# Kernel tuning notes

Hardware: AMD Instinct MI355X
Metric: run time of the kernel (lower is better)

Reference implementation:

```python
import jax, jax.numpy as jnp
import numpy as np

B, S, D, H = 2, 2048, 1024, 16
DK = D // H


def setup_inputs() -> dict:
    key = jax.random.key(0)
    ks = jax.random.split(key, 11)
    scale = 1.0 / np.sqrt(D)
    inp = {
        'q': jax.random.normal(ks[0], (B, S, D), jnp.float32),
        'k': jax.random.normal(ks[1], (B, S, D), jnp.float32),
        'v': jax.random.normal(ks[2], (B, S, D), jnp.float32),
        'mask': jnp.tril(jnp.ones((S, S), jnp.int32))[None, None],  # [1,1,S,S] causal
        'w_q': jax.random.normal(ks[3], (D, D), jnp.float32) * scale,
        'b_q': jax.random.normal(ks[4], (D,), jnp.float32) * scale,
        'w_k': jax.random.normal(ks[5], (D, D), jnp.float32) * scale,
        'b_k': jax.random.normal(ks[6], (D,), jnp.float32) * scale,
        'w_v': jax.random.normal(ks[7], (D, D), jnp.float32) * scale,
        'b_v': jax.random.normal(ks[8], (D,), jnp.float32) * scale,
        'w_o': jax.random.normal(ks[9], (D, D), jnp.float32) * scale,
        'b_o': jax.random.normal(ks[10], (D,), jnp.float32) * scale,
    }
    return inp


def reference(q, k, v, mask, w_q, b_q, w_k, b_k, w_v, b_v, w_o, b_o):
    # Linear projections (torch Linear: x @ W^T + b; here weights stored as [D_in, D_out])
    query = q @ w_q + b_q  # [B,S,D]
    key_ = k @ w_k + b_k
    value = v @ w_v + b_v
    # split heads -> [B,H,S,DK]
    def split(x):
        return x.reshape(B, S, H, DK).transpose(0, 2, 1, 3)
    qh, kh, vh = split(query), split(key_), split(value)
    scores = jnp.einsum('bhqd,bhkd->bhqk', qh, kh) / jnp.sqrt(jnp.float32(DK))
    scores = jnp.where(mask == 0, jnp.float32(-1e9), scores)
    attn = jax.nn.softmax(scores, axis=-1)  # dropout p=0.0 -> identity
    out = jnp.einsum('bhqk,bhkd->bhqd', attn, vh)  # [B,H,S,DK]
    out = out.transpose(0, 2, 1, 3).reshape(B, S, D)
    return out @ w_o + b_o
```

## Files before the change

kernel.cpp:

```cpp
#include <hip/hip_runtime.h>

typedef unsigned short u16;
typedef unsigned int u32;
typedef __attribute__((ext_vector_type(8))) short short8;
typedef __attribute__((ext_vector_type(4))) float f32x4;
typedef __attribute__((ext_vector_type(4))) float float4v;
typedef __attribute__((ext_vector_type(4))) u16 u16x4;
typedef __attribute__((ext_vector_type(2))) u32 u32x2;

#define DEV static __device__ __forceinline__

static constexpr int S_LEN = 2048;
static constexpr int D_MODEL = 1024;
static constexpr int N_HEADS = 16;
static constexpr int DK = 64;
static constexpr float LOG2E = 1.4426950408889634f;
static constexpr float SM_SHIFT = 12.0f;

#if defined(__has_builtin)
#if __has_builtin(__builtin_amdgcn_exp2f)
#define EXP2(x) __builtin_amdgcn_exp2f(x)
#else
#define EXP2(x) exp2f(x)
#endif
#else
#define EXP2(x) exp2f(x)
#endif

DEV u16 f2bf(float f) {
  u32 u = __builtin_bit_cast(u32, f);
  u32 r = (u + 0x7FFFu + ((u >> 16) & 1u)) >> 16;
  return (u16)r;
}

DEV u32 pk2bf(float lo, float hi) {
  u32 d;
  asm("v_cvt_pk_bf16_f32 %0, %1, %2" : "=v"(d) : "v"(lo), "v"(hi));
  return d;
}

DEV void async16(const void* g, void* l) {
  __builtin_amdgcn_global_load_lds(
      (const __attribute__((address_space(1))) u32*)g,
      (__attribute__((address_space(3))) u32*)l, 16, 0, 0);
}

DEV short8 lds_frag(const u16* tile, int row, int byteInRow) {
  const char* p = (const char*)tile + row * 128 + (byteInRow ^ ((row & 7) << 4));
  return *(const short8*)p;
}

DEV f32x4 mfma16(short8 a, short8 b, f32x4 c) {
  return __builtin_amdgcn_mfma_f32_16x16x32_bf16(a, b, c, 0, 0, 0);
}

__global__ void k_cvt3(const float* __restrict__ q, const float* __restrict__ k,
                       const float* __restrict__ v, u16* __restrict__ xq,
                       u16* __restrict__ xk, u16* __restrict__ xv, int n) {
  const float* src = blockIdx.y == 0 ? q : (blockIdx.y == 1 ? k : v);
  u16* dst = blockIdx.y == 0 ? xq : (blockIdx.y == 1 ? xk : xv);
  int i = (blockIdx.x * blockDim.x + threadIdx.x) * 4;
  int stride = gridDim.x * blockDim.x * 4;
  for (; i < n; i += stride) {
    float4v f = *(const float4v*)(src + i);
    u16x4 o;
    o[0] = f2bf(f[0]); o[1] = f2bf(f[1]); o[2] = f2bf(f[2]); o[3] = f2bf(f[3]);
    *(u16x4*)(dst + i) = o;
  }
}

__global__ void k_twz4(const float* __restrict__ wq, const float* __restrict__ wk,
                       const float* __restrict__ wv, const float* __restrict__ wo,
                       u16* __restrict__ tq, u16* __restrict__ tk,
                       u16* __restrict__ tv, u16* __restrict__ to_) {
  __shared__ u16 t[64][65];
  const int z = blockIdx.z;
  const float* W = z == 0 ? wq : (z == 1 ? wk : (z == 2 ? wv : wo));
  u16* Wt = z == 0 ? tq : (z == 1 ? tk : (z == 2 ? tv : to_));
  const int n0 = blockIdx.x * 64;
  const int k0 = blockIdx.y * 64;
  const int tid = threadIdx.x;
  const int c = tid & 63, r0 = tid >> 6;
#pragma unroll
  for (int j = 0; j < 16; ++j) {
    int r = r0 + j * 4;
    t[r][c] = f2bf(W[(size_t)(k0 + r) * D_MODEL + n0 + c]);
  }
  __syncthreads();
#pragma unroll
  for (int j = 0; j < 16; ++j) {
    int r = r0 + j * 4;
    Wt[(size_t)(n0 + r) * D_MODEL + k0 + c] = t[c][r];
  }
}

__global__ __launch_bounds__(256, 2) void k_gemm3(
    const u16* __restrict__ Xq, const u16* __restrict__ Xk, const u16* __restrict__ Xv,
    const u16* __restrict__ Wtq, const u16* __restrict__ Wtk, const u16* __restrict__ Wtv,
    const float* __restrict__ bq, const float* __restrict__ bk, const float* __restrict__ bv,
    u16* __restrict__ Qh, u16* __restrict__ Kh, u16* __restrict__ Vtp) {
  const int z = blockIdx.z;
  const u16* A = z == 0 ? Xq : (z == 1 ? Xk : Xv);
  const u16* Bt = z == 0 ? Wtq : (z == 1 ? Wtk : Wtv);
  const float* bias = z == 0 ? bq : (z == 1 ? bk : bv);
  u16* obf = z == 0 ? Qh : (z == 1 ? Kh : Vtp);
  const float scale = z == 0 ? 0.125f * LOG2E : 1.0f;

  __shared__ __align__(16) u16 As[128 * 64];
  __shared__ __align__(16) u16 Bs[128 * 64];
  const int tid = threadIdx.x;
  const int lane = tid & 63, w = tid >> 6;
  const int l15 = lane & 15, l4 = lane >> 4;
  const int bm = blockIdx.x * 128, bn = blockIdx.y * 128;
  const int wr = (w >> 1) * 64, wc = (w & 1) * 64;
  const int sr = tid >> 3, sc8 = tid & 7;
  f32x4 acc[4][4] = {};

  for (int k0 = 0; k0 < 1024; k0 += 64) {
    __syncthreads();
#pragma unroll
    for (int j = 0; j < 4; ++j) {
      int row = sr + j * 32;
      int col = (sc8 ^ (row & 7)) << 3;
      async16(A + (size_t)(bm + row) * 1024 + k0 + col, (char*)As + tid * 16 + j * 4096);
      async16(Bt + (size_t)(bn + row) * 1024 + k0 + col, (char*)Bs + tid * 16 + j * 4096);
    }
    __syncthreads();
    short8 af[4][2], bfv[4][2];
#pragma unroll
    for (int mi = 0; mi < 4; ++mi)
#pragma unroll
      for (int kk = 0; kk < 2; ++kk)
        af[mi][kk] = lds_frag(As, wr + mi * 16 + l15, kk * 64 + l4 * 16);
#pragma unroll
    for (int ni = 0; ni < 4; ++ni)
#pragma unroll
      for (int kk = 0; kk < 2; ++kk)
        bfv[ni][kk] = lds_frag(Bs, wc + ni * 16 + l15, kk * 64 + l4 * 16);
#pragma unroll
    for (int kk = 0; kk < 2; ++kk)
#pragma unroll
      for (int mi = 0; mi < 4; ++mi)
#pragma unroll
        for (int ni = 0; ni < 4; ++ni)
          acc[mi][ni] = mfma16(af[mi][kk], bfv[ni][kk], acc[mi][ni]);
  }

#pragma unroll
  for (int mi = 0; mi < 4; ++mi)
#pragma unroll
    for (int ni = 0; ni < 4; ++ni) {
      const int row0 = bm + wr + mi * 16 + l4 * 4;
      const int col = bn + wc + ni * 16 + l15;
      const int h = col >> 6, dk = col & 63;
      const int b = row0 >> 11, s0 = row0 & 2047;
      if (z == 2) {
        u16x4 pk;
#pragma unroll
        for (int r = 0; r < 4; ++r) pk[r] = f2bf(acc[mi][ni][r] + bias[col]);
        *(u16x4*)(obf + ((size_t)((b * N_HEADS + h) * DK + dk)) * S_LEN + s0) = pk;
      } else {
#pragma unroll
        for (int r = 0; r < 4; ++r) {
          float vv = (acc[mi][ni][r] + bias[col]) * scale;
          obf[(((size_t)(b * N_HEADS + h) * S_LEN + s0 + r) << 6) + dk] = f2bf(vv);
        }
      }
    }
}

__global__ __launch_bounds__(256, 2) void k_gemmO(
    const u16* __restrict__ A, const u16* __restrict__ Bt,
    const float* __restrict__ bias, float* __restrict__ ofp) {
  __shared__ __align__(16) u16 As[128 * 64];
  __shared__ __align__(16) u16 Bs[64 * 64];
  const int tid = threadIdx.x;
  const int lane = tid & 63, w = tid >> 6;
  const int l15 = lane & 15, l4 = lane >> 4;
  const int bm = blockIdx.x * 128, bn = blockIdx.y * 64;
  const int wr = w * 32;
  const int sr = tid >> 3, sc8 = tid & 7;
  f32x4 acc[2][4] = {};

  for (int k0 = 0; k0 < 1024; k0 += 64) {
    __syncthreads();
#pragma unroll
    for (int j = 0; j < 4; ++j) {
      int row = sr + j * 32;
      int col = (sc8 ^ (row & 7)) << 3;
      async16(A + (size_t)(bm + row) * 1024 + k0 + col, (char*)As + tid * 16 + j * 4096);
      if (j < 2)
        async16(Bt + (size_t)(bn + row) * 1024 + k0 + col, (char*)Bs + tid * 16 + j * 4096);
    }
    __syncthreads();
    short8 af[2][2], bfv[4][2];
#pragma unroll
    for (int mi = 0; mi < 2; ++mi)
#pragma unroll
      for (int kk = 0; kk < 2; ++kk)
        af[mi][kk] = lds_frag(As, wr + mi * 16 + l15, kk * 64 + l4 * 16);
#pragma unroll
    for (int ni = 0; ni < 4; ++ni)
#pragma unroll
      for (int kk = 0; kk < 2; ++kk)
        bfv[ni][kk] = lds_frag(Bs, ni * 16 + l15, kk * 64 + l4 * 16);
#pragma unroll
    for (int kk = 0; kk < 2; ++kk)
#pragma unroll
      for (int mi = 0; mi < 2; ++mi)
#pragma unroll
        for (int ni = 0; ni < 4; ++ni)
          acc[mi][ni] = mfma16(af[mi][kk], bfv[ni][kk], acc[mi][ni]);
  }

#pragma unroll
  for (int mi = 0; mi < 2; ++mi)
#pragma unroll
    for (int ni = 0; ni < 4; ++ni)
#pragma unroll
      for (int r = 0; r < 4; ++r) {
        int row = bm + wr + mi * 16 + l4 * 4 + r;
        int col = bn + ni * 16 + l15;
        ofp[(size_t)row * D_MODEL + col] = acc[mi][ni][r] + bias[col];
      }
}

__global__ __launch_bounds__(256, 4) void k_attn(
    const u16* __restrict__ Qh, const u16* __restrict__ Kh,
    const u16* __restrict__ Vt, u16* __restrict__ Om) {
  __shared__ __align__(16) u16 Ks[2][64 * 64];
  __shared__ __align__(16) u16 Vs[2][64 * 64];
  __shared__ __align__(16) u16 Ps[4][16 * 64];
  const int tid = threadIdx.x;
  const int lane = tid & 63, w = tid >> 6;
  const int l15 = lane & 15, l4 = lane >> 4;
  const int bh = blockIdx.x;
  const int jq = 31 - (int)blockIdx.y;
  const int q0 = jq * 64;
  const int qw = q0 + w * 16;
  const u16* Qb = Qh + (size_t)bh * S_LEN * DK;
  const u16* Kb = Kh + (size_t)bh * S_LEN * DK;
  const u16* Vb = Vt + (size_t)bh * DK * S_LEN;
  const int sr = tid >> 3, sc8 = tid & 7;
  const int b = bh >> 4, h = bh & 15;
  u16* Pw = Ps[w];

  auto stage = [&](int t0, int buf) {
#pragma unroll
    for (int j = 0; j < 2; ++j) {
      int row = sr + j * 32;
      int col = (sc8 ^ (row & 7)) << 3;
      async16(Kb + (size_t)(t0 + row) * DK + col, (char*)Ks[buf] + tid * 16 + j * 4096);
      async16(Vb + (size_t)row * S_LEN + t0 + col, (char*)Vs[buf] + tid * 16 + j * 4096);
    }
  };

  short8 qf[2];
#pragma unroll
  for (int kk = 0; kk < 2; ++kk)
    qf[kk] = *(const short8*)(Qb + (size_t)(qw + l15) * DK + kk * 32 + l4 * 8);

  f32x4 o[4] = {};
  float rs = 0.f;
  const int nt = jq + 1;

  stage(0, 0);
  __syncthreads();
  int cur = 0;
#pragma unroll 1
  for (int ti = 0; ti < nt; ++ti) {
    const int t0 = ti << 6;
    if (ti + 1 < nt) stage(t0 + 64, cur ^ 1);

    f32x4 sf[4];
#pragma unroll
    for (int mi = 0; mi < 4; ++mi)
#pragma unroll
      for (int r = 0; r < 4; ++r) sf[mi][r] = -SM_SHIFT;
    __builtin_amdgcn_s_setprio(1);
#pragma unroll
    for (int kk = 0; kk < 2; ++kk)
#pragma unroll
      for (int mi = 0; mi < 4; ++mi) {
        short8 kf = lds_frag(Ks[cur], mi * 16 + l15, kk * 64 + l4 * 16);
        sf[mi] = mfma16(kf, qf[kk], sf[mi]);
      }
    __builtin_amdgcn_s_setprio(0);

    if (t0 + 63 > qw) {
      const int qrow = qw + l15;
#pragma unroll
      for (int mi = 0; mi < 4; ++mi)
#pragma unroll
        for (int r = 0; r < 4; ++r)
          if (t0 + mi * 16 + l4 * 4 + r > qrow) sf[mi][r] = -1e30f;
    }

#pragma unroll
    for (int mi = 0; mi < 4; ++mi) {
      float p0 = EXP2(sf[mi][0]);
      float p1 = EXP2(sf[mi][1]);
      float p2 = EXP2(sf[mi][2]);
      float p3 = EXP2(sf[mi][3]);
      rs += (p0 + p1) + (p2 + p3);
      u32x2 pk;
      pk[0] = pk2bf(p0, p1);
      pk[1] = pk2bf(p2, p3);
      *(u32x2*)((char*)Pw + l15 * 128 + ((mi * 32 + l4 * 8) ^ ((l15 & 7) << 4))) = pk;
    }

    __builtin_amdgcn_s_setprio(1);
#pragma unroll
    for (int kk = 0; kk < 2; ++kk) {
      short8 pf = lds_frag(Pw, l15, kk * 64 + l4 * 16);
#pragma unroll
      for (int ni = 0; ni < 4; ++ni) {
        short8 vf = lds_frag(Vs[cur], ni * 16 + l15, kk * 64 + l4 * 16);
        o[ni] = mfma16(pf, vf, o[ni]);
      }
    }
    __builtin_amdgcn_s_setprio(0);
    __syncthreads();
    cur ^= 1;
  }

  rs += __shfl_xor(rs, 16);
  rs += __shfl_xor(rs, 32);
  f32x4 lv;
#pragma unroll
  for (int r = 0; r < 4; ++r) lv[r] = __shfl(rs, l4 * 4 + r);

#pragma unroll
  for (int ni = 0; ni < 4; ++ni)
#pragma unroll
    for (int r = 0; r < 4; ++r) {
      int s = qw + l4 * 4 + r;
      int d = ni * 16 + l15;
      Om[(size_t)(b * S_LEN + s) * D_MODEL + h * DK + d] = f2bf(o[ni][r] / lv[r]);
    }
}

extern "C" void kernel_launch(void* const* d_in, const int* in_sizes, int n_in,
                              void* d_out, int out_size, void* d_ws, size_t ws_size,
                              hipStream_t stream) {
  (void)in_sizes; (void)n_in; (void)out_size; (void)ws_size;
  const float* q  = (const float*)d_in[0];
  const float* k  = (const float*)d_in[1];
  const float* v  = (const float*)d_in[2];
  const float* wq = (const float*)d_in[4];
  const float* bq = (const float*)d_in[5];
  const float* wk = (const float*)d_in[6];
  const float* bk = (const float*)d_in[7];
  const float* wv = (const float*)d_in[8];
  const float* bv = (const float*)d_in[9];
  const float* wo = (const float*)d_in[10];
  const float* bo = (const float*)d_in[11];
  float* out = (float*)d_out;

  char* ws = (char*)d_ws;
  const size_t XB = (size_t)4096 * 1024 * 2;
  const size_t WB = (size_t)1024 * 1024 * 2;
  u16* Xq  = (u16*)(ws);
  u16* Xk  = (u16*)(ws + XB);
  u16* Xv  = (u16*)(ws + 2 * XB);
  u16* Wtq = (u16*)(ws + 3 * XB);
  u16* Wtk = (u16*)(ws + 3 * XB + WB);
  u16* Wtv = (u16*)(ws + 3 * XB + 2 * WB);
  u16* Wto = (u16*)(ws + 3 * XB + 3 * WB);
  u16* Qh  = (u16*)(ws + 3 * XB + 4 * WB);
  u16* Kh  = (u16*)(ws + 4 * XB + 4 * WB);
  u16* Vtp = (u16*)(ws + 5 * XB + 4 * WB);
  u16* Om  = Xq;

  const int n = 4096 * 1024;
  k_cvt3<<<dim3(512, 3), 256, 0, stream>>>(q, k, v, Xq, Xk, Xv, n);
  k_twz4<<<dim3(16, 16, 4), 256, 0, stream>>>(wq, wk, wv, wo, Wtq, Wtk, Wtv, Wto);
  k_gemm3<<<dim3(32, 8, 3), 256, 0, stream>>>(Xq, Xk, Xv, Wtq, Wtk, Wtv,
                                              bq, bk, bv, Qh, Kh, Vtp);
  k_attn<<<dim3(32, 32), 256, 0, stream>>>(Qh, Kh, Vtp, Om);
  k_gemmO<<<dim3(32, 16), 256, 0, stream>>>(Om, Wto, bo, out);
}
```

Measured before the change: 109.8 us.

## Split long causal attention rows across two blocks and combine partials

The attention kernel now uses 512-thread blocks covering 128 query rows. Query groups in the second half of the sequence are split along the key axis into two partial blocks, which write unnormalized outputs and row sums to workspace. A new combine kernel sums the two partials and normalizes them. The aim is to balance the causal triangle's uneven work across blocks and reduce tail imbalance, at the cost of an extra launch and fp32 partial traffic. Because the softmax uses a fixed shift rather than a running max, the partials can simply be added.

```diff
diff --git a/kernel.cpp b/kernel.cpp
--- a/kernel.cpp
+++ b/kernel.cpp
@@ -225,34 +225,43 @@
       }
 }
 
-__global__ __launch_bounds__(256, 4) void k_attn(
+__global__ __launch_bounds__(512, 6) void k_attn(
     const u16* __restrict__ Qh, const u16* __restrict__ Kh,
-    const u16* __restrict__ Vt, u16* __restrict__ Om) {
+    const u16* __restrict__ Vt, u16* __restrict__ Om,
+    float* __restrict__ Po, float* __restrict__ Pl) {
   __shared__ __align__(16) u16 Ks[2][64 * 64];
   __shared__ __align__(16) u16 Vs[2][64 * 64];
-  __shared__ __align__(16) u16 Ps[4][16 * 64];
+  __shared__ __align__(16) u16 Ps[8][16 * 64];
   const int tid = threadIdx.x;
   const int lane = tid & 63, w = tid >> 6;
   const int l15 = lane & 15, l4 = lane >> 4;
-  const int bh = blockIdx.x;
-  const int jq = 31 - (int)blockIdx.y;
-  const int q0 = jq * 64;
-  const int qw = q0 + w * 16;
+  const int bid = blockIdx.x;
+
+  int bh, g, c, tbeg, tend;
+  bool partial;
+  if (bid < 256) {
+    bh = bid & 31; g = 8 + (bid >> 5); c = 0; tbeg = 0; tend = 16; partial = true;
+  } else if (bid < 512) {
+    int i = bid - 256;
+    bh = i & 31; g = 15 - (i >> 5); c = 1; tbeg = 16; tend = 2 * g + 2; partial = true;
+  } else {
+    int i = bid - 512;
+    bh = i & 31; g = 7 - (i >> 5); c = 0; tbeg = 0; tend = 2 * g + 2; partial = false;
+  }
+
   const u16* Qb = Qh + (size_t)bh * S_LEN * DK;
   const u16* Kb = Kh + (size_t)bh * S_LEN * DK;
   const u16* Vb = Vt + (size_t)bh * DK * S_LEN;
-  const int sr = tid >> 3, sc8 = tid & 7;
-  const int b = bh >> 4, h = bh & 15;
+  const int q0 = g * 128;
+  const int qw = q0 + w * 16;
+  const int sc8 = tid & 7;
   u16* Pw = Ps[w];
 
   auto stage = [&](int t0, int buf) {
-#pragma unroll
-    for (int j = 0; j < 2; ++j) {
-      int row = sr + j * 32;
-      int col = (sc8 ^ (row & 7)) << 3;
-      async16(Kb + (size_t)(t0 + row) * DK + col, (char*)Ks[buf] + tid * 16 + j * 4096);
-      async16(Vb + (size_t)row * S_LEN + t0 + col, (char*)Vs[buf] + tid * 16 + j * 4096);
-    }
+    int row = tid >> 3;
+    int col = (sc8 ^ (row & 7)) << 3;
+    async16(Kb + (size_t)(t0 + row) * DK + col, (char*)Ks[buf] + tid * 16);
+    async16(Vb + (size_t)row * S_LEN + t0 + col, (char*)Vs[buf] + tid * 16);
   };
 
   short8 qf[2];
@@ -262,15 +271,14 @@
 
   f32x4 o[4] = {};
   float rs = 0.f;
-  const int nt = jq + 1;
-
-  stage(0, 0);
+
+  stage(tbeg << 6, 0);
   __syncthreads();
   int cur = 0;
 #pragma unroll 1
-  for (int ti = 0; ti < nt; ++ti) {
+  for (int ti = tbeg; ti < tend; ++ti) {
     const int t0 = ti << 6;
-    if (ti + 1 < nt) stage(t0 + 64, cur ^ 1);
+    if (ti + 1 < tend) stage((ti + 1) << 6, cur ^ 1);
 
     f32x4 sf[4];
 #pragma unroll
@@ -326,18 +334,55 @@
 
   rs += __shfl_xor(rs, 16);
   rs += __shfl_xor(rs, 32);
-  f32x4 lv;
-#pragma unroll
-  for (int r = 0; r < 4; ++r) lv[r] = __shfl(rs, l4 * 4 + r);
-
-#pragma unroll
-  for (int ni = 0; ni < 4; ++ni)
-#pragma unroll
-    for (int r = 0; r < 4; ++r) {
-      int s = qw + l4 * 4 + r;
-      int d = ni * 16 + l15;
-      Om[(size_t)(b * S_LEN + s) * D_MODEL + h * DK + d] = f2bf(o[ni][r] / lv[r]);
-    }
+
+  if (partial) {
+    const int slot = ((bh << 3) + (g - 8)) * 2 + c;
+    float* PoS = Po + (size_t)slot * (128 * 64);
+#pragma unroll
+    for (int ni = 0; ni < 4; ++ni)
+#pragma unroll
+      for (int r = 0; r < 4; ++r)
+        PoS[(w * 16 + l4 * 4 + r) * 64 + ni * 16 + l15] = o[ni][r];
+    if (l4 == 0) Pl[slot * 128 + w * 16 + l15] = rs;
+  } else {
+    f32x4 lv;
+#pragma unroll
+    for (int r = 0; r < 4; ++r) lv[r] = __shfl(rs, l4 * 4 + r);
+    const int b = bh >> 4, h = bh & 15;
+#pragma unroll
+    for (int ni = 0; ni < 4; ++ni)
+#pragma unroll
+      for (int r = 0; r < 4; ++r) {
+        int s = qw + l4 * 4 + r;
+        int d = ni * 16 + l15;
+        Om[(size_t)(b * S_LEN + s) * D_MODEL + h * DK + d] = f2bf(o[ni][r] / lv[r]);
+      }
+  }
+}
+
+__global__ void k_comb(const float* __restrict__ Po, const float* __restrict__ Pl,
+                       u16* __restrict__ Om) {
+  const int bh = blockIdx.x, g8 = blockIdx.y;
+  const int tid = threadIdx.x;
+  const int slot0 = ((bh << 3) + g8) * 2;
+  const float* P0 = Po + (size_t)slot0 * (128 * 64);
+  const float* P1 = P0 + (128 * 64);
+  const float* L0 = Pl + slot0 * 128;
+  const float* L1 = L0 + 128;
+  const int b = bh >> 4, h = bh & 15;
+  const int row0 = tid >> 4, c4 = (tid & 15) * 4;
+#pragma unroll
+  for (int j = 0; j < 8; ++j) {
+    int row = j * 16 + row0;
+    float4v a = *(const float4v*)(P0 + row * 64 + c4);
+    float4v bb = *(const float4v*)(P1 + row * 64 + c4);
+    float inv = 1.f / (L0[row] + L1[row]);
+    u16x4 ov;
+#pragma unroll
+    for (int i = 0; i < 4; ++i) ov[i] = f2bf((a[i] + bb[i]) * inv);
+    int s = 1024 + g8 * 128 + row;
+    *(u16x4*)(Om + (size_t)(b * S_LEN + s) * D_MODEL + h * DK + c4) = ov;
+  }
 }
 
 extern "C" void kernel_launch(void* const* d_in, const int* in_sizes, int n_in,
@@ -370,6 +415,8 @@
   u16* Qh  = (u16*)(ws + 3 * XB + 4 * WB);
   u16* Kh  = (u16*)(ws + 4 * XB + 4 * WB);
   u16* Vtp = (u16*)(ws + 5 * XB + 4 * WB);
+  float* Po = (float*)(ws + XB);
+  float* Pl = (float*)(ws + 6 * XB + 4 * WB);
   u16* Om  = Xq;
 
   const int n = 4096 * 1024;
@@ -377,6 +424,7 @@
   k_twz4<<<dim3(16, 16, 4), 256, 0, stream>>>(wq, wk, wv, wo, Wtq, Wtk, Wtv, Wto);
   k_gemm3<<<dim3(32, 8, 3), 256, 0, stream>>>(Xq, Xk, Xv, Wtq, Wtk, Wtv,
                                               bq, bk, bv, Qh, Kh, Vtp);
-  k_attn<<<dim3(32, 32), 256, 0, stream>>>(Qh, Kh, Vtp, Om);
+  k_attn<<<768, 512, 0, stream>>>(Qh, Kh, Vtp, Om, Po, Pl);
+  k_comb<<<dim3(32, 8), 256, 0, stream>>>(Po, Pl, Om);
   k_gemmO<<<dim3(32, 16), 256, 0, stream>>>(Om, Wto, bo, out);
 }
```

Result: no change. 111.8 us (+1.9%).

## Merge prep kernels and remap workgroup order for XCD locality and causal balance

Applied to the files above, without the earlier changes.

Fuses the activation conversion and weight transpose kernels into one launch, removing a kernel boundary. Remaps the linear block index in both projection GEMMs so that consecutive blocks dispatched round-robin to the 8 XCDs handle neighbouring tiles, which should improve L2 reuse. Reorders causal attention query tiles so heavy and light tiles interleave across dispatch, balancing load. Some prep blocks are launched only to exit immediately, and the remap assumes specific grid sizes.

```diff
diff --git a/kernel.cpp b/kernel.cpp
--- a/kernel.cpp
+++ b/kernel.cpp
@@ -54,43 +54,46 @@
   return __builtin_amdgcn_mfma_f32_16x16x32_bf16(a, b, c, 0, 0, 0);
 }
 
-__global__ void k_cvt3(const float* __restrict__ q, const float* __restrict__ k,
-                       const float* __restrict__ v, u16* __restrict__ xq,
-                       u16* __restrict__ xk, u16* __restrict__ xv, int n) {
-  const float* src = blockIdx.y == 0 ? q : (blockIdx.y == 1 ? k : v);
-  u16* dst = blockIdx.y == 0 ? xq : (blockIdx.y == 1 ? xk : xv);
-  int i = (blockIdx.x * blockDim.x + threadIdx.x) * 4;
-  int stride = gridDim.x * blockDim.x * 4;
-  for (; i < n; i += stride) {
-    float4v f = *(const float4v*)(src + i);
-    u16x4 o;
-    o[0] = f2bf(f[0]); o[1] = f2bf(f[1]); o[2] = f2bf(f[2]); o[3] = f2bf(f[3]);
-    *(u16x4*)(dst + i) = o;
-  }
-}
-
-__global__ void k_twz4(const float* __restrict__ wq, const float* __restrict__ wk,
+__global__ void k_prep(const float* __restrict__ q, const float* __restrict__ k,
+                       const float* __restrict__ v,
+                       const float* __restrict__ wq, const float* __restrict__ wk,
                        const float* __restrict__ wv, const float* __restrict__ wo,
+                       u16* __restrict__ xq, u16* __restrict__ xk, u16* __restrict__ xv,
                        u16* __restrict__ tq, u16* __restrict__ tk,
                        u16* __restrict__ tv, u16* __restrict__ to_) {
   __shared__ u16 t[64][65];
-  const int z = blockIdx.z;
-  const float* W = z == 0 ? wq : (z == 1 ? wk : (z == 2 ? wv : wo));
-  u16* Wt = z == 0 ? tq : (z == 1 ? tk : (z == 2 ? tv : to_));
-  const int n0 = blockIdx.x * 64;
-  const int k0 = blockIdx.y * 64;
-  const int tid = threadIdx.x;
-  const int c = tid & 63, r0 = tid >> 6;
-#pragma unroll
-  for (int j = 0; j < 16; ++j) {
-    int r = r0 + j * 4;
-    t[r][c] = f2bf(W[(size_t)(k0 + r) * D_MODEL + n0 + c]);
-  }
-  __syncthreads();
-#pragma unroll
-  for (int j = 0; j < 16; ++j) {
-    int r = r0 + j * 4;
-    Wt[(size_t)(n0 + r) * D_MODEL + k0 + c] = t[c][r];
+  const int z = blockIdx.y;
+  if (z < 3) {
+    const float* src = z == 0 ? q : (z == 1 ? k : v);
+    u16* dst = z == 0 ? xq : (z == 1 ? xk : xv);
+    int i = (blockIdx.x * 256 + threadIdx.x) * 4;
+    const int stride = 512 * 256 * 4;
+    for (; i < 4096 * 1024; i += stride) {
+      float4v f = *(const float4v*)(src + i);
+      u16x4 o;
+      o[0] = f2bf(f[0]); o[1] = f2bf(f[1]); o[2] = f2bf(f[2]); o[3] = f2bf(f[3]);
+      *(u16x4*)(dst + i) = o;
+    }
+  } else {
+    if (blockIdx.x >= 256) return;
+    const int zz = z - 3;
+    const float* W = zz == 0 ? wq : (zz == 1 ? wk : (zz == 2 ? wv : wo));
+    u16* Wt = zz == 0 ? tq : (zz == 1 ? tk : (zz == 2 ? tv : to_));
+    const int n0 = (blockIdx.x & 15) * 64;
+    const int k0 = (blockIdx.x >> 4) * 64;
+    const int tid = threadIdx.x;
+    const int c = tid & 63, r0 = tid >> 6;
+#pragma unroll
+    for (int j = 0; j < 16; ++j) {
+      int r = r0 + j * 4;
+      t[r][c] = f2bf(W[(size_t)(k0 + r) * D_MODEL + n0 + c]);
+    }
+    __syncthreads();
+#pragma unroll
+    for (int j = 0; j < 16; ++j) {
+      int r = r0 + j * 4;
+      Wt[(size_t)(n0 + r) * D_MODEL + k0 + c] = t[c][r];
+    }
   }
 }
 
@@ -99,7 +102,10 @@
     const u16* __restrict__ Wtq, const u16* __restrict__ Wtk, const u16* __restrict__ Wtv,
     const float* __restrict__ bq, const float* __restrict__ bk, const float* __restrict__ bv,
     u16* __restrict__ Qh, u16* __restrict__ Kh, u16* __restrict__ Vtp) {
-  const int z = blockIdx.z;
+  const int lin = blockIdx.x + (blockIdx.y << 5) + (blockIdx.z << 8);
+  const int wg = (lin & 7) * 96 + (lin >> 3);
+  const int bx = wg & 31, by = (wg >> 5) & 7;
+  const int z = wg >> 8;
   const u16* A = z == 0 ? Xq : (z == 1 ? Xk : Xv);
   const u16* Bt = z == 0 ? Wtq : (z == 1 ? Wtk : Wtv);
   const float* bias = z == 0 ? bq : (z == 1 ? bk : bv);
@@ -111,7 +117,7 @@
   const int tid = threadIdx.x;
   const int lane = tid & 63, w = tid >> 6;
   const int l15 = lane & 15, l4 = lane >> 4;
-  const int bm = blockIdx.x * 128, bn = blockIdx.y * 128;
+  const int bm = bx * 128, bn = by * 128;
   const int wr = (w >> 1) * 64, wc = (w & 1) * 64;
   const int sr = tid >> 3, sc8 = tid & 7;
   f32x4 acc[4][4] = {};
@@ -172,12 +178,15 @@
 __global__ __launch_bounds__(256, 2) void k_gemmO(
     const u16* __restrict__ A, const u16* __restrict__ Bt,
     const float* __restrict__ bias, float* __restrict__ ofp) {
+  const int lin = blockIdx.x + (blockIdx.y << 5);
+  const int wg = (lin & 7) * 64 + (lin >> 3);
+  const int bx = wg & 31, by = wg >> 5;
   __shared__ __align__(16) u16 As[128 * 64];
   __shared__ __align__(16) u16 Bs[64 * 64];
   const int tid = threadIdx.x;
   const int lane = tid & 63, w = tid >> 6;
   const int l15 = lane & 15, l4 = lane >> 4;
-  const int bm = blockIdx.x * 128, bn = blockIdx.y * 64;
+  const int bm = bx * 128, bn = by * 64;
   const int wr = w * 32;
   const int sr = tid >> 3, sc8 = tid & 7;
   f32x4 acc[2][4] = {};
@@ -235,7 +244,8 @@
   const int lane = tid & 63, w = tid >> 6;
   const int l15 = lane & 15, l4 = lane >> 4;
   const int bh = blockIdx.x;
-  const int jq = 31 - (int)blockIdx.y;
+  const int y = blockIdx.y, y0 = y & 7, qd = y >> 3;
+  const int jq = qd == 0 ? y0 : (qd == 1 ? 31 - y0 : (qd == 2 ? 8 + y0 : 23 - y0));
   const int q0 = jq * 64;
   const int qw = q0 + w * 16;
   const u16* Qb = Qh + (size_t)bh * S_LEN * DK;
@@ -372,9 +382,8 @@
   u16* Vtp = (u16*)(ws + 5 * XB + 4 * WB);
   u16* Om  = Xq;
 
-  const int n = 4096 * 1024;
-  k_cvt3<<<dim3(512, 3), 256, 0, stream>>>(q, k, v, Xq, Xk, Xv, n);
-  k_twz4<<<dim3(16, 16, 4), 256, 0, stream>>>(wq, wk, wv, wo, Wtq, Wtk, Wtv, Wto);
+  k_prep<<<dim3(512, 7), 256, 0, stream>>>(q, k, v, wq, wk, wv, wo,
+                                           Xq, Xk, Xv, Wtq, Wtk, Wtv, Wto);
   k_gemm3<<<dim3(32, 8, 3), 256, 0, stream>>>(Xq, Xk, Xv, Wtq, Wtk, Wtv,
                                               bq, bk, bv, Qh, Kh, Vtp);
   k_attn<<<dim3(32, 32), 256, 0, stream>>>(Qh, Kh, Vtp, Om);
```

After: 108.3 us. About the same (-1.3%).
